# Performance work log

Hardware: AMD Instinct MI355X
Metric: run time of the kernel (lower is better)

The kernel has to match this reference:

```python
import jax, jax.numpy as jnp
import numpy as np

D_MODEL = 2048
N_HEADS = 16
HEAD_DIM = D_MODEL // N_HEADS


def setup_inputs() -> dict:
    key = jax.random.key(0)
    ks = jax.random.split(key, 5)
    scale = 1.0 / np.sqrt(D_MODEL)
    x = jax.random.normal(ks[0], (2, 2048, D_MODEL), dtype=jnp.float32)
    W_qkv = jax.random.normal(ks[1], (D_MODEL, 3 * D_MODEL), dtype=jnp.float32) * scale
    b_qkv = jnp.zeros((3 * D_MODEL,), dtype=jnp.float32)
    W_out = jax.random.normal(ks[2], (D_MODEL, D_MODEL), dtype=jnp.float32) * scale
    b_out = jnp.zeros((D_MODEL,), dtype=jnp.float32)
    return {"x": x, "W_qkv": W_qkv, "b_qkv": b_qkv, "W_out": W_out, "b_out": b_out}


def reference(x, W_qkv, b_qkv, W_out, b_out):
    bsz, seq_len, _ = x.shape
    # QKV projection: (b, s, 3*d) -> (3, b, h, s, hd)
    qkv = x @ W_qkv + b_qkv
    qkv = qkv.reshape(bsz, seq_len, 3, N_HEADS, HEAD_DIM)
    qkv = jnp.transpose(qkv, (2, 0, 3, 1, 4))
    q, k, v = qkv[0], qkv[1], qkv[2]
    # scaled dot-product scores: (b, h, s, s)
    scores = jnp.einsum("bhqd,bhkd->bhqk", q, k) / np.sqrt(HEAD_DIM).astype(np.float32)
    causal = jnp.tril(jnp.ones((seq_len, seq_len), dtype=bool))
    scores = jnp.where(causal[None, None], scores, -jnp.inf)
    attn = jax.nn.softmax(scores, axis=-1)
    # attention output: (b, h, s, hd) -> (b, s, d)
    out = jnp.einsum("bhqk,bhkd->bhqd", attn, v)
    out = jnp.transpose(out, (0, 2, 1, 3)).reshape(bsz, seq_len, D_MODEL)
    y = out @ W_out + b_out
    return y
```

## Files before the change

### kernel.cpp

```cpp
#include <hip/hip_runtime.h>
#include <stdint.h>
#include <stddef.h>


typedef __attribute__((ext_vector_type(8))) short bf16x8;
typedef __attribute__((ext_vector_type(4))) float f32x4;

#define SOFT_SCALE 0.12751743075419806f

__device__ __forceinline__ short f2bf(float f) {
  union { float f; unsigned u; } v; v.f = f;
  unsigned u = v.u + 0x7fffu + ((v.u >> 16) & 1u);
  return (short)(u >> 16);
}

__device__ __forceinline__ void gload_lds16(const void* g, const void* l) {
  __builtin_amdgcn_global_load_lds(
      (__attribute__((address_space(1))) void*)(uintptr_t)g,
      (__attribute__((address_space(3))) void*)(uintptr_t)l,
      16, 0, 0);
}

__global__ __launch_bounds__(256) void cast_f32_bf16(
    const float* __restrict__ in, short* __restrict__ out, int n8) {
  int i = blockIdx.x * 256 + threadIdx.x;
  if (i >= n8) return;
  float4 a = ((const float4*)in)[i * 2];
  float4 b = ((const float4*)in)[i * 2 + 1];
  bf16x8 o;
  o[0] = f2bf(a.x); o[1] = f2bf(a.y); o[2] = f2bf(a.z); o[3] = f2bf(a.w);
  o[4] = f2bf(b.x); o[5] = f2bf(b.y); o[6] = f2bf(b.z); o[7] = f2bf(b.w);
  ((bf16x8*)out)[i] = o;
}

__global__ __launch_bounds__(256) void transpose_cast_w(
    const float* __restrict__ W, short* __restrict__ WT, int K, int N) {
  __shared__ short t[32][33];
  int k0 = blockIdx.x * 32, n0 = blockIdx.y * 32;
  int r = threadIdx.x >> 3;
  int c = (threadIdx.x & 7) * 4;
  float4 v = *(const float4*)(W + (size_t)(k0 + r) * N + n0 + c);
  t[r][c + 0] = f2bf(v.x); t[r][c + 1] = f2bf(v.y);
  t[r][c + 2] = f2bf(v.z); t[r][c + 3] = f2bf(v.w);
  __syncthreads();
  short4 o;
  o.x = t[c + 0][r]; o.y = t[c + 1][r]; o.z = t[c + 2][r]; o.w = t[c + 3][r];
  *(short4*)(WT + (size_t)(n0 + r) * K + k0 + c) = o;
}

template <int BF16OUT, int VTRANS, int QSCALE>
__global__ __launch_bounds__(512, 2) void gemm256(
    const short* __restrict__ A, const short* __restrict__ BT,
    void* __restrict__ Cv, const float* __restrict__ bias,
    short* __restrict__ vTout, int M, int N, int K) {
  (void)M;
  __shared__ __align__(16) short SH[73728];
  const int tid = threadIdx.x;
  const int wave = tid >> 6, lane = tid & 63;
  const int quad = lane >> 4, l16 = lane & 15;
  const int wm = wave >> 1, wn = wave & 1;
  const int kx = (l16 & 7) << 3;

  const int gx = gridDim.x;
  int bid = blockIdx.y * gx + blockIdx.x;
  const int nwg = gx * gridDim.y;
  bid = (bid & 7) * (nwg >> 3) + (bid >> 3);
  const int m0 = (bid % gx) * 256, n0 = (bid / gx) * 128;

  const int rsub = lane >> 3;
  const int csub = ((lane & 7) ^ rsub) << 3;
  const short* aS[4];
  const short* bS[2];
#pragma unroll
  for (int i = 0; i < 4; ++i)
    aS[i] = A + (size_t)(m0 + (wave * 4 + i) * 8 + rsub) * K + csub;
#pragma unroll
  for (int i = 0; i < 2; ++i)
    bS[i] = BT + (size_t)(n0 + (wave * 2 + i) * 8 + rsub) * K + csub;

  auto stageA = [&](int st, int sb) {
#pragma unroll
    for (int i = 0; i < 4; ++i)
      gload_lds16(aS[i] + st * 64,
                  (const char*)SH + sb * 49152 + (wave * 4 + i) * 1024);
  };
  auto stageB = [&](int st, int sb) {
#pragma unroll
    for (int i = 0; i < 2; ++i)
      gload_lds16(bS[i] + st * 64,
                  (const char*)SH + sb * 49152 + 32768 + (wave * 2 + i) * 1024);
  };

  stageA(0, 0); stageB(0, 0);
  stageA(1, 1); stageB(1, 1);

  f32x4 acc[4][4] = {};
  const int nT = K >> 6;
  int buf = 0, sb = 2;
  for (int t = 0; t < nT; ++t) {
    const int st = (t + 2 < nT) ? (t + 2) : (nT - 1);
    const short* As = (const short*)((const char*)SH + buf * 49152);
    const short* Bs = As + 16384;

    asm volatile("s_waitcnt vmcnt(6)" ::: "memory");
    __builtin_amdgcn_s_barrier();

    bf16x8 af[4][2], bf[2][2];
#pragma unroll
    for (int f = 0; f < 4; ++f) {
      const int row = wm * 64 + f * 16 + l16;
#pragma unroll
      for (int kk = 0; kk < 2; ++kk)
        af[f][kk] = *(const bf16x8*)(As + row * 64 +
                                     (((kk << 5) | (quad << 3)) ^ kx));
    }
#pragma unroll
    for (int u = 0; u < 2; ++u) {
      const int row = wn * 64 + u * 16 + l16;
#pragma unroll
      for (int kk = 0; kk < 2; ++kk)
        bf[u][kk] = *(const bf16x8*)(Bs + row * 64 +
                                     (((kk << 5) | (quad << 3)) ^ kx));
    }
    stageA(st, sb);
    __builtin_amdgcn_s_barrier();
    asm volatile("s_waitcnt lgkmcnt(0)" ::: "memory");
    __builtin_amdgcn_sched_barrier(0);
    __builtin_amdgcn_s_setprio(1);
#pragma unroll
    for (int f = 0; f < 4; ++f)
#pragma unroll
      for (int u = 0; u < 2; ++u)
#pragma unroll
        for (int kk = 0; kk < 2; ++kk)
          acc[f][u] = __builtin_amdgcn_mfma_f32_16x16x32_bf16(
              af[f][kk], bf[u][kk], acc[f][u], 0, 0, 0);
    __builtin_amdgcn_s_setprio(0);
    __builtin_amdgcn_s_barrier();

#pragma unroll
    for (int u = 0; u < 2; ++u) {
      const int row = wn * 64 + 32 + u * 16 + l16;
#pragma unroll
      for (int kk = 0; kk < 2; ++kk)
        bf[u][kk] = *(const bf16x8*)(Bs + row * 64 +
                                     (((kk << 5) | (quad << 3)) ^ kx));
    }
    stageB(st, sb);
    __builtin_amdgcn_s_barrier();
    asm volatile("s_waitcnt lgkmcnt(0)" ::: "memory");
    __builtin_amdgcn_sched_barrier(0);
    __builtin_amdgcn_s_setprio(1);
#pragma unroll
    for (int f = 0; f < 4; ++f)
#pragma unroll
      for (int u = 0; u < 2; ++u)
#pragma unroll
        for (int kk = 0; kk < 2; ++kk)
          acc[f][2 + u] = __builtin_amdgcn_mfma_f32_16x16x32_bf16(
              af[f][kk], bf[u][kk], acc[f][2 + u], 0, 0, 0);
    __builtin_amdgcn_s_setprio(0);

    buf = (buf == 2) ? 0 : buf + 1;
    sb = (sb == 2) ? 0 : sb + 1;
  }

  if (VTRANS && n0 >= 4096) {
    asm volatile("s_waitcnt vmcnt(0)" ::: "memory");
    __builtin_amdgcn_s_barrier();
    short* T = (short*)SH;
#pragma unroll
    for (int j = 0; j < 4; ++j) {
      const int nl = wn * 64 + j * 16 + l16;
      const float bv = bias[n0 + nl];
#pragma unroll
      for (int f = 0; f < 4; ++f) {
        const int ml = wm * 64 + f * 16 + quad * 4;
        short4 o;
        o.x = f2bf(acc[f][j][0] + bv);
        o.y = f2bf(acc[f][j][1] + bv);
        o.z = f2bf(acc[f][j][2] + bv);
        o.w = f2bf(acc[f][j][3] + bv);
        *(short4*)(T + nl * 264 + ml) = o;
      }
    }
    __builtin_amdgcn_s_barrier();
    const int b = m0 >> 11, s0 = m0 & 2047, h = (n0 - 4096) >> 7;
#pragma unroll
    for (int pass = 0; pass < 8; ++pass) {
      const int row = pass * 16 + (tid >> 5);
      const int c = (tid & 31) * 8;
      bf16x8 v = *(const bf16x8*)(T + row * 264 + c);
      *(bf16x8*)(vTout + ((size_t)((b * 16 + h) * 128 + row)) * 2048 + s0 +
                 c) = v;
    }
    return;
  }

#pragma unroll
  for (int j = 0; j < 4; ++j) {
    const int n = n0 + wn * 64 + j * 16 + l16;
    const float bv = bias[n];
#pragma unroll
    for (int f = 0; f < 4; ++f) {
      const int mb = m0 + wm * 64 + f * 16 + quad * 4;
#pragma unroll
      for (int r = 0; r < 4; ++r) {
        float v = acc[f][j][r] + bv;
        if (QSCALE && n < 2048) v *= SOFT_SCALE;
        if (BF16OUT)
          ((short*)Cv)[(size_t)(mb + r) * N + n] = f2bf(v);
        else
          ((float*)Cv)[(size_t)(mb + r) * N + n] = v;
      }
    }
  }
}

__global__ __launch_bounds__(512, 4) void attn_kernel(
    const short* __restrict__ qkv, const short* __restrict__ vT,
    short* __restrict__ obuf) {
  __shared__ __align__(16) short Ks[2 * 8192];
  __shared__ __align__(16) short Vs[2 * 8192];
  __shared__ __align__(16) short Ps[8192];
  const int tid = threadIdx.x;
  const int wave = tid >> 6, lane = tid & 63;
  const int quad = lane >> 4, l16 = lane & 15;
  const int bh = blockIdx.y, b = bh >> 4, h = bh & 15;
  const int px = blockIdx.x;
  const int p = (blockIdx.y & 16) ? (15 - px) : px;
  const int q0 = p * 128;
  const int nkt = 2 * (p + 1);

  const short* qbase = qkv + (size_t)b * 2048 * 6144 + h * 128;
  const short* kbase = qkv + (size_t)b * 2048 * 6144 + 2048 + h * 128;
  const short* vtbase = vT + (size_t)bh * 128 * 2048;
  short* obase = obuf + (size_t)b * 2048 * 2048 + h * 128;

  const int srow = lane >> 2;
  const int scol = (lane & 3) * 8;

  bf16x8 ones;
#pragma unroll
  for (int j = 0; j < 8; ++j) ones[j] = (short)0x3F80;

  bf16x8 qf[4];
#pragma unroll
  for (int kk = 0; kk < 4; ++kk)
    qf[kk] = *(const bf16x8*)(
        qbase + (size_t)(q0 + wave * 16 + l16) * 6144 + kk * 32 + quad * 8);

  f32x4 acco[8] = {};
  f32x4 accl = {};

  auto stage = [&](int buf, int kt) {
    const int k0 = kt * 64;
#pragma unroll
    for (int it = 0; it < 2; ++it) {
      int c = wave * 2 + it;
      gload_lds16(
          kbase + (size_t)(k0 + (c & 3) * 16 + srow) * 6144 + (c >> 2) * 32 +
              scol,
          (const char*)Ks + buf * 16384 + c * 1024);
    }
#pragma unroll
    for (int it = 0; it < 2; ++it) {
      int c = wave * 2 + it;
      gload_lds16(
          vtbase + (size_t)((c & 7) * 16 + srow) * 2048 + k0 + (c >> 3) * 32 +
              scol,
          (const char*)Vs + buf * 16384 + c * 1024);
    }
  };

  stage(0, 0);

  for (int kt = 0; kt < nkt; ++kt) {
    const int buf = kt & 1;
    __syncthreads();
    if (kt + 1 < nkt) stage(1 - buf, kt + 1);
    const short* KsB = Ks + buf * 8192;
    const short* VsB = Vs + buf * 8192;

    f32x4 accs[4] = {};
#pragma unroll
    for (int kk = 0; kk < 4; ++kk) {
      bf16x8 bfg[4];
#pragma unroll
      for (int tn = 0; tn < 4; ++tn)
        bfg[tn] = *(const bf16x8*)(KsB + (kk * 4 + tn) * 512 + l16 * 32 +
                                   quad * 8);
#pragma unroll
      for (int tn = 0; tn < 4; ++tn)
        accs[tn] = __builtin_amdgcn_mfma_f32_16x16x32_bf16(
            qf[kk], bfg[tn], accs[tn], 0, 0, 0);
    }

    if (kt >= nkt - 2) {
      const int k0 = kt * 64;
#pragma unroll
      for (int tn = 0; tn < 4; ++tn)
#pragma unroll
        for (int r = 0; r < 4; ++r) {
          int grow = q0 + wave * 16 + quad * 4 + r;
          int gcol = k0 + tn * 16 + l16;
          if (gcol > grow) accs[tn][r] = -1e30f;
        }
    }
#pragma unroll
    for (int tn = 0; tn < 4; ++tn)
#pragma unroll
      for (int r = 0; r < 4; ++r) accs[tn][r] = exp2f(accs[tn][r]);

#pragma unroll
    for (int r = 0; r < 4; ++r)
#pragma unroll
      for (int tn = 0; tn < 4; ++tn)
        Ps[wave * 1024 + (tn >> 1) * 512 + (quad * 4 + r) * 32 +
           (tn & 1) * 16 + l16] = f2bf(accs[tn][r]);

#pragma unroll
    for (int kk2 = 0; kk2 < 2; ++kk2) {
      bf16x8 av = *(const bf16x8*)(Ps + wave * 1024 + kk2 * 512 + l16 * 32 +
                                   quad * 8);
      accl = __builtin_amdgcn_mfma_f32_16x16x32_bf16(av, ones, accl, 0, 0, 0);
      bf16x8 bfg[8];
#pragma unroll
      for (int tn = 0; tn < 8; ++tn)
        bfg[tn] = *(const bf16x8*)(VsB + (kk2 * 8 + tn) * 512 + l16 * 32 +
                                   quad * 8);
#pragma unroll
      for (int tn = 0; tn < 8; ++tn)
        acco[tn] = __builtin_amdgcn_mfma_f32_16x16x32_bf16(
            av, bfg[tn], acco[tn], 0, 0, 0);
    }
  }

  float inv[4];
#pragma unroll
  for (int r = 0; r < 4; ++r) inv[r] = 1.f / accl[r];
#pragma unroll
  for (int r = 0; r < 4; ++r) {
    int row = q0 + wave * 16 + quad * 4 + r;
#pragma unroll
    for (int tn = 0; tn < 8; ++tn)
      obase[(size_t)row * 2048 + tn * 16 + l16] = f2bf(acco[tn][r] * inv[r]);
  }
}

extern "C" void kernel_launch(void* const* d_in, const int* in_sizes, int n_in,
                              void* d_out, int out_size, void* d_ws,
                              size_t ws_size, hipStream_t stream) {
  (void)in_sizes; (void)n_in; (void)out_size; (void)ws_size;
  const float* x    = (const float*)d_in[0];
  const float* Wqkv = (const float*)d_in[1];
  const float* bqkv = (const float*)d_in[2];
  const float* Wout = (const float*)d_in[3];
  const float* bout = (const float*)d_in[4];
  float* out = (float*)d_out;

  char* ws = (char*)d_ws;
  short* xb    = (short*)(ws);
  short* wqkvT = (short*)(ws + 16777216);
  short* woutT = (short*)(ws + 41943040);
  short* qkv   = (short*)(ws + 50331648);
  short* vTb   = (short*)(ws + 100663296);
  short* obuf  = (short*)(ws + 117440512);

  cast_f32_bf16<<<4096, 256, 0, stream>>>(x, xb, 1048576);
  transpose_cast_w<<<dim3(64, 192), 256, 0, stream>>>(Wqkv, wqkvT, 2048, 6144);
  transpose_cast_w<<<dim3(64, 64), 256, 0, stream>>>(Wout, woutT, 2048, 2048);

  gemm256<1, 1, 1><<<dim3(16, 48), 512, 0, stream>>>(
      xb, wqkvT, (void*)qkv, bqkv, vTb, 4096, 6144, 2048);

  attn_kernel<<<dim3(16, 32), 512, 0, stream>>>(qkv, vTb, obuf);

  gemm256<0, 0, 0><<<dim3(16, 16), 512, 0, stream>>>(
      obuf, woutT, (void*)out, bout, nullptr, 4096, 2048, 2048);
}
```

Baseline: 363.6 us.

## Give each attention wave two query row groups and XOR-swizzle LDS tiles

```diff
diff --git a/kernel.cpp b/kernel.cpp
--- a/kernel.cpp
+++ b/kernel.cpp
@@ -217,7 +217,7 @@
   }
 }
 
-__global__ __launch_bounds__(512, 4) void attn_kernel(
+__global__ __launch_bounds__(256, 2) void attn_kernel(
     const short* __restrict__ qkv, const short* __restrict__ vT,
     short* __restrict__ obuf) {
   __shared__ __align__(16) short Ks[2 * 8192];
@@ -238,34 +238,38 @@
   short* obase = obuf + (size_t)b * 2048 * 2048 + h * 128;
 
   const int srow = lane >> 2;
-  const int scol = (lane & 3) * 8;
+  const int scol = ((lane & 3) ^ (srow & 3)) * 8;
+  const int kx = ((l16 & 3) << 3);
 
   bf16x8 ones;
 #pragma unroll
   for (int j = 0; j < 8; ++j) ones[j] = (short)0x3F80;
 
-  bf16x8 qf[4];
-#pragma unroll
-  for (int kk = 0; kk < 4; ++kk)
-    qf[kk] = *(const bf16x8*)(
-        qbase + (size_t)(q0 + wave * 16 + l16) * 6144 + kk * 32 + quad * 8);
-
-  f32x4 acco[8] = {};
-  f32x4 accl = {};
+  bf16x8 qf[2][4];
+#pragma unroll
+  for (int rg = 0; rg < 2; ++rg)
+#pragma unroll
+    for (int kk = 0; kk < 4; ++kk)
+      qf[rg][kk] = *(const bf16x8*)(
+          qbase + (size_t)(q0 + wave * 32 + rg * 16 + l16) * 6144 + kk * 32 +
+          quad * 8);
+
+  f32x4 acco[2][8] = {};
+  f32x4 accl[2] = {};
 
   auto stage = [&](int buf, int kt) {
     const int k0 = kt * 64;
 #pragma unroll
-    for (int it = 0; it < 2; ++it) {
-      int c = wave * 2 + it;
+    for (int it = 0; it < 4; ++it) {
+      int c = wave * 4 + it;
       gload_lds16(
           kbase + (size_t)(k0 + (c & 3) * 16 + srow) * 6144 + (c >> 2) * 32 +
               scol,
           (const char*)Ks + buf * 16384 + c * 1024);
     }
 #pragma unroll
-    for (int it = 0; it < 2; ++it) {
-      int c = wave * 2 + it;
+    for (int it = 0; it < 4; ++it) {
+      int c = wave * 4 + it;
       gload_lds16(
           vtbase + (size_t)((c & 7) * 16 + srow) * 2048 + k0 + (c >> 3) * 32 +
               scol,
@@ -282,70 +286,90 @@
     const short* KsB = Ks + buf * 8192;
     const short* VsB = Vs + buf * 8192;
 
-    f32x4 accs[4] = {};
+    f32x4 accs[2][4] = {};
 #pragma unroll
     for (int kk = 0; kk < 4; ++kk) {
       bf16x8 bfg[4];
 #pragma unroll
       for (int tn = 0; tn < 4; ++tn)
         bfg[tn] = *(const bf16x8*)(KsB + (kk * 4 + tn) * 512 + l16 * 32 +
-                                   quad * 8);
-#pragma unroll
-      for (int tn = 0; tn < 4; ++tn)
-        accs[tn] = __builtin_amdgcn_mfma_f32_16x16x32_bf16(
-            qf[kk], bfg[tn], accs[tn], 0, 0, 0);
+                                   ((quad * 8) ^ kx));
+#pragma unroll
+      for (int rg = 0; rg < 2; ++rg)
+#pragma unroll
+        for (int tn = 0; tn < 4; ++tn)
+          accs[rg][tn] = __builtin_amdgcn_mfma_f32_16x16x32_bf16(
+              qf[rg][kk], bfg[tn], accs[rg][tn], 0, 0, 0);
     }
 
     if (kt >= nkt - 2) {
       const int k0 = kt * 64;
 #pragma unroll
+      for (int rg = 0; rg < 2; ++rg)
+#pragma unroll
+        for (int tn = 0; tn < 4; ++tn)
+#pragma unroll
+          for (int r = 0; r < 4; ++r) {
+            int grow = q0 + wave * 32 + rg * 16 + quad * 4 + r;
+            int gcol = k0 + tn * 16 + l16;
+            if (gcol > grow) accs[rg][tn][r] = -1e30f;
+          }
+    }
+#pragma unroll
+    for (int rg = 0; rg < 2; ++rg)
+#pragma unroll
       for (int tn = 0; tn < 4; ++tn)
 #pragma unroll
-        for (int r = 0; r < 4; ++r) {
-          int grow = q0 + wave * 16 + quad * 4 + r;
-          int gcol = k0 + tn * 16 + l16;
-          if (gcol > grow) accs[tn][r] = -1e30f;
+        for (int r = 0; r < 4; ++r) accs[rg][tn][r] = exp2f(accs[rg][tn][r]);
+
+#pragma unroll
+    for (int rg = 0; rg < 2; ++rg)
+#pragma unroll
+      for (int r = 0; r < 4; ++r)
+#pragma unroll
+        for (int tn = 0; tn < 4; ++tn) {
+          const int row = rg * 16 + quad * 4 + r;
+          const int col = (tn & 1) * 16 + l16;
+          const int pcol = (col & 7) | ((((col >> 3) ^ row) & 3) << 3);
+          Ps[wave * 2048 + (tn >> 1) * 1024 + row * 32 + pcol] =
+              f2bf(accs[rg][tn][r]);
         }
-    }
-#pragma unroll
-    for (int tn = 0; tn < 4; ++tn)
-#pragma unroll
-      for (int r = 0; r < 4; ++r) accs[tn][r] = exp2f(accs[tn][r]);
-
-#pragma unroll
-    for (int r = 0; r < 4; ++r)
-#pragma unroll
-      for (int tn = 0; tn < 4; ++tn)
-        Ps[wave * 1024 + (tn >> 1) * 512 + (quad * 4 + r) * 32 +
-           (tn & 1) * 16 + l16] = f2bf(accs[tn][r]);
 
 #pragma unroll
     for (int kk2 = 0; kk2 < 2; ++kk2) {
-      bf16x8 av = *(const bf16x8*)(Ps + wave * 1024 + kk2 * 512 + l16 * 32 +
-                                   quad * 8);
-      accl = __builtin_amdgcn_mfma_f32_16x16x32_bf16(av, ones, accl, 0, 0, 0);
+      bf16x8 av[2];
+#pragma unroll
+      for (int rg = 0; rg < 2; ++rg)
+        av[rg] = *(const bf16x8*)(Ps + wave * 2048 + kk2 * 1024 +
+                                  (rg * 16 + l16) * 32 + ((quad * 8) ^ kx));
+#pragma unroll
+      for (int rg = 0; rg < 2; ++rg)
+        accl[rg] = __builtin_amdgcn_mfma_f32_16x16x32_bf16(av[rg], ones,
+                                                           accl[rg], 0, 0, 0);
       bf16x8 bfg[8];
 #pragma unroll
       for (int tn = 0; tn < 8; ++tn)
         bfg[tn] = *(const bf16x8*)(VsB + (kk2 * 8 + tn) * 512 + l16 * 32 +
-                                   quad * 8);
+                                   ((quad * 8) ^ kx));
 #pragma unroll
       for (int tn = 0; tn < 8; ++tn)
-        acco[tn] = __builtin_amdgcn_mfma_f32_16x16x32_bf16(
-            av, bfg[tn], acco[tn], 0, 0, 0);
+#pragma unroll
+        for (int rg = 0; rg < 2; ++rg)
+          acco[rg][tn] = __builtin_amdgcn_mfma_f32_16x16x32_bf16(
+              av[rg], bfg[tn], acco[rg][tn], 0, 0, 0);
     }
   }
 
-  float inv[4];
-#pragma unroll
-  for (int r = 0; r < 4; ++r) inv[r] = 1.f / accl[r];
-#pragma unroll
-  for (int r = 0; r < 4; ++r) {
-    int row = q0 + wave * 16 + quad * 4 + r;
-#pragma unroll
-    for (int tn = 0; tn < 8; ++tn)
-      obase[(size_t)row * 2048 + tn * 16 + l16] = f2bf(acco[tn][r] * inv[r]);
-  }
+#pragma unroll
+  for (int rg = 0; rg < 2; ++rg)
+#pragma unroll
+    for (int r = 0; r < 4; ++r) {
+      const float inv = 1.f / accl[rg][r];
+      const int row = q0 + wave * 32 + rg * 16 + quad * 4 + r;
+#pragma unroll
+      for (int tn = 0; tn < 8; ++tn)
+        obase[(size_t)row * 2048 + tn * 16 + l16] = f2bf(acco[rg][tn][r] * inv);
+    }
 }
 
 extern "C" void kernel_launch(void* const* d_in, const int* in_sizes, int n_in,
@@ -374,7 +398,7 @@
   gemm256<1, 1, 1><<<dim3(16, 48), 512, 0, stream>>>(
       xb, wqkvT, (void*)qkv, bqkv, vTb, 4096, 6144, 2048);
 
-  attn_kernel<<<dim3(16, 32), 512, 0, stream>>>(qkv, vTb, obuf);
+  attn_kernel<<<dim3(16, 32), 256, 0, stream>>>(qkv, vTb, obuf);
 
   gemm256<0, 0, 0><<<dim3(16, 16), 512, 0, stream>>>(
       obuf, woutT, (void*)out, bout, nullptr, 4096, 2048, 2048);
```

Measured after the change: 369.1 us. No clear change (+1.5%).

## Use dedicated 256x256-tile QKV GEMM with double-buffered staged loads

Applied to the files above, without the earlier changes.

```diff
diff --git a/kernel.cpp b/kernel.cpp
--- a/kernel.cpp
+++ b/kernel.cpp
@@ -48,11 +48,218 @@
   *(short4*)(WT + (size_t)(n0 + r) * K + k0 + c) = o;
 }
 
-template <int BF16OUT, int VTRANS, int QSCALE>
-__global__ __launch_bounds__(512, 2) void gemm256(
+__global__ __launch_bounds__(512, 2) void gemm_qkv(
     const short* __restrict__ A, const short* __restrict__ BT,
-    void* __restrict__ Cv, const float* __restrict__ bias,
+    short* __restrict__ C, const float* __restrict__ bias,
     short* __restrict__ vTout, int M, int N, int K) {
+  (void)M;
+  __shared__ __align__(16) short SH[66048];
+  const int tid = threadIdx.x;
+  const int wave = tid >> 6, lane = tid & 63;
+  const int quad = lane >> 4, l16 = lane & 15;
+  const int wm = wave >> 2, wn = wave & 3;
+  const int kx = (l16 & 7) << 3;
+
+  const int gx = gridDim.x;
+  int bid = blockIdx.y * gx + blockIdx.x;
+  const int nwg = gx * gridDim.y;
+  bid = (bid & 7) * (nwg >> 3) + (bid >> 3);
+  const int m0 = (bid % gx) * 256, n0 = (bid / gx) * 256;
+
+  const int rsub = lane >> 3;
+  const int csub = ((lane & 7) ^ rsub) << 3;
+  const int e1 = (wave & 3) + 8 * (wave >> 2);
+  const int cA[4] = {wave, wave + 16, wave + 8, wave + 24};
+  const int cB[4] = {e1, e1 + 16, e1 + 4, e1 + 20};
+  const short* aP[4];
+  const short* bP[4];
+#pragma unroll
+  for (int i = 0; i < 4; ++i) {
+    aP[i] = A + (size_t)(m0 + cA[i] * 8 + rsub) * K + csub;
+    bP[i] = BT + (size_t)(n0 + cB[i] * 8 + rsub) * K + csub;
+  }
+
+  auto stage = [&](int h, int st, int sbuf) {
+    if (h == 0 || h == 2) {
+      int i0 = (h == 0) ? 0 : 2;
+#pragma unroll
+      for (int i = 0; i < 2; ++i)
+        gload_lds16(aP[i0 + i] + st * 64,
+                    (const char*)SH + sbuf * 65536 + cA[i0 + i] * 1024);
+    } else {
+      int i0 = (h == 1) ? 0 : 2;
+#pragma unroll
+      for (int i = 0; i < 2; ++i)
+        gload_lds16(bP[i0 + i] + st * 64,
+                    (const char*)SH + sbuf * 65536 + 32768 + cB[i0 + i] * 1024);
+    }
+  };
+
+  stage(0, 0, 0); stage(1, 0, 0); stage(2, 0, 0); stage(3, 0, 0);
+
+  f32x4 acc[8][4] = {};
+  const int nT = K >> 6;
+  for (int t = 0; t < nT; ++t) {
+    const int st = (t + 1 < nT) ? (t + 1) : (nT - 1);
+    const int sbuf = (t + 1) & 1;
+    const short* As = SH + (t & 1) * 32768;
+    const short* Bs = As + 16384;
+    bf16x8 bf[4][2];
+
+    asm volatile("s_waitcnt vmcnt(4)" ::: "memory");
+    __builtin_amdgcn_s_barrier();
+    bf16x8 af0[4][2];
+#pragma unroll
+    for (int f = 0; f < 4; ++f) {
+      const int row = wm * 128 + f * 16 + l16;
+#pragma unroll
+      for (int kk = 0; kk < 2; ++kk)
+        af0[f][kk] = *(const bf16x8*)(As + row * 64 +
+                                      (((kk << 5) | (quad << 3)) ^ kx));
+    }
+#pragma unroll
+    for (int u = 0; u < 2; ++u) {
+      const int row = wn * 64 + u * 16 + l16;
+#pragma unroll
+      for (int kk = 0; kk < 2; ++kk)
+        bf[u][kk] = *(const bf16x8*)(Bs + row * 64 +
+                                     (((kk << 5) | (quad << 3)) ^ kx));
+    }
+    stage(0, st, sbuf);
+    __builtin_amdgcn_s_barrier();
+    asm volatile("s_waitcnt lgkmcnt(0)" ::: "memory");
+    __builtin_amdgcn_sched_barrier(0);
+    __builtin_amdgcn_s_setprio(1);
+#pragma unroll
+    for (int f = 0; f < 4; ++f)
+#pragma unroll
+      for (int u = 0; u < 2; ++u)
+#pragma unroll
+        for (int kk = 0; kk < 2; ++kk)
+          acc[f][u] = __builtin_amdgcn_mfma_f32_16x16x32_bf16(
+              af0[f][kk], bf[u][kk], acc[f][u], 0, 0, 0);
+    __builtin_amdgcn_s_setprio(0);
+
+    asm volatile("s_waitcnt vmcnt(2)" ::: "memory");
+    __builtin_amdgcn_s_barrier();
+#pragma unroll
+    for (int u = 0; u < 2; ++u) {
+      const int row = wn * 64 + 32 + u * 16 + l16;
+#pragma unroll
+      for (int kk = 0; kk < 2; ++kk)
+        bf[2 + u][kk] = *(const bf16x8*)(Bs + row * 64 +
+                                         (((kk << 5) | (quad << 3)) ^ kx));
+    }
+    stage(1, st, sbuf);
+    __builtin_amdgcn_s_barrier();
+    asm volatile("s_waitcnt lgkmcnt(0)" ::: "memory");
+    __builtin_amdgcn_sched_barrier(0);
+    __builtin_amdgcn_s_setprio(1);
+#pragma unroll
+    for (int f = 0; f < 4; ++f)
+#pragma unroll
+      for (int u = 0; u < 2; ++u)
+#pragma unroll
+        for (int kk = 0; kk < 2; ++kk)
+          acc[f][2 + u] = __builtin_amdgcn_mfma_f32_16x16x32_bf16(
+              af0[f][kk], bf[2 + u][kk], acc[f][2 + u], 0, 0, 0);
+    __builtin_amdgcn_s_setprio(0);
+
+    __builtin_amdgcn_s_barrier();
+    bf16x8 af1[4][2];
+#pragma unroll
+    for (int f = 0; f < 4; ++f) {
+      const int row = wm * 128 + 64 + f * 16 + l16;
+#pragma unroll
+      for (int kk = 0; kk < 2; ++kk)
+        af1[f][kk] = *(const bf16x8*)(As + row * 64 +
+                                      (((kk << 5) | (quad << 3)) ^ kx));
+    }
+    stage(2, st, sbuf);
+    __builtin_amdgcn_s_barrier();
+    asm volatile("s_waitcnt lgkmcnt(0)" ::: "memory");
+    __builtin_amdgcn_sched_barrier(0);
+    __builtin_amdgcn_s_setprio(1);
+#pragma unroll
+    for (int f = 0; f < 4; ++f)
+#pragma unroll
+      for (int u = 0; u < 2; ++u)
+#pragma unroll
+        for (int kk = 0; kk < 2; ++kk)
+          acc[4 + f][u] = __builtin_amdgcn_mfma_f32_16x16x32_bf16(
+              af1[f][kk], bf[u][kk], acc[4 + f][u], 0, 0, 0);
+    __builtin_amdgcn_s_setprio(0);
+
+    __builtin_amdgcn_s_barrier();
+    stage(3, st, sbuf);
+    __builtin_amdgcn_s_setprio(1);
+#pragma unroll
+    for (int f = 0; f < 4; ++f)
+#pragma unroll
+      for (int u = 0; u < 2; ++u)
+#pragma unroll
+        for (int kk = 0; kk < 2; ++kk)
+          acc[4 + f][2 + u] = __builtin_amdgcn_mfma_f32_16x16x32_bf16(
+              af1[f][kk], bf[2 + u][kk], acc[4 + f][2 + u], 0, 0, 0);
+    __builtin_amdgcn_s_setprio(0);
+  }
+
+  asm volatile("s_waitcnt vmcnt(0)" ::: "memory");
+  __builtin_amdgcn_s_barrier();
+
+  if (n0 >= 4096) {
+    short* T = (short*)SH;
+#pragma unroll
+    for (int j = 0; j < 4; ++j) {
+      const int nl = wn * 64 + j * 16 + l16;
+      const float bv = bias[n0 + nl];
+#pragma unroll
+      for (int f = 0; f < 8; ++f) {
+        const int ml = wm * 128 + f * 16 + quad * 4;
+        short4 o;
+        o.x = f2bf(acc[f][j][0] + bv);
+        o.y = f2bf(acc[f][j][1] + bv);
+        o.z = f2bf(acc[f][j][2] + bv);
+        o.w = f2bf(acc[f][j][3] + bv);
+        *(short4*)(T + nl * 258 + ml) = o;
+      }
+    }
+    __builtin_amdgcn_s_barrier();
+    const int b = m0 >> 11, s0 = m0 & 2047, h0 = (n0 - 4096) >> 7;
+#pragma unroll
+    for (int pass = 0; pass < 16; ++pass) {
+      const int nl = pass * 16 + (tid >> 5);
+      const int c = (tid & 31) * 8;
+      bf16x8 v = *(const bf16x8*)(T + nl * 258 + c);
+      *(bf16x8*)(vTout +
+                 ((size_t)((b * 16 + h0 + (nl >> 7)) * 128 + (nl & 127))) *
+                     2048 +
+                 s0 + c) = v;
+    }
+    return;
+  }
+
+#pragma unroll
+  for (int j = 0; j < 4; ++j) {
+    const int n = n0 + wn * 64 + j * 16 + l16;
+    const float bv = bias[n];
+#pragma unroll
+    for (int f = 0; f < 8; ++f) {
+      const int mb = m0 + wm * 128 + f * 16 + quad * 4;
+#pragma unroll
+      for (int r = 0; r < 4; ++r) {
+        float v = acc[f][j][r] + bv;
+        if (n < 2048) v *= SOFT_SCALE;
+        C[(size_t)(mb + r) * N + n] = f2bf(v);
+      }
+    }
+  }
+}
+
+__global__ __launch_bounds__(512, 2) void gemm_out(
+    const short* __restrict__ A, const short* __restrict__ BT,
+    float* __restrict__ C, const float* __restrict__ bias, int M, int N,
+    int K) {
   (void)M;
   __shared__ __align__(16) short SH[73728];
   const int tid = threadIdx.x;
@@ -165,37 +372,7 @@
     sb = (sb == 2) ? 0 : sb + 1;
   }
 
-  if (VTRANS && n0 >= 4096) {
-    asm volatile("s_waitcnt vmcnt(0)" ::: "memory");
-    __builtin_amdgcn_s_barrier();
-    short* T = (short*)SH;
-#pragma unroll
-    for (int j = 0; j < 4; ++j) {
-      const int nl = wn * 64 + j * 16 + l16;
-      const float bv = bias[n0 + nl];
-#pragma unroll
-      for (int f = 0; f < 4; ++f) {
-        const int ml = wm * 64 + f * 16 + quad * 4;
-        short4 o;
-        o.x = f2bf(acc[f][j][0] + bv);
-        o.y = f2bf(acc[f][j][1] + bv);
-        o.z = f2bf(acc[f][j][2] + bv);
-        o.w = f2bf(acc[f][j][3] + bv);
-        *(short4*)(T + nl * 264 + ml) = o;
-      }
-    }
-    __builtin_amdgcn_s_barrier();
-    const int b = m0 >> 11, s0 = m0 & 2047, h = (n0 - 4096) >> 7;
-#pragma unroll
-    for (int pass = 0; pass < 8; ++pass) {
-      const int row = pass * 16 + (tid >> 5);
-      const int c = (tid & 31) * 8;
-      bf16x8 v = *(const bf16x8*)(T + row * 264 + c);
-      *(bf16x8*)(vTout + ((size_t)((b * 16 + h) * 128 + row)) * 2048 + s0 +
-                 c) = v;
-    }
-    return;
-  }
+  asm volatile("s_waitcnt vmcnt(0)" ::: "memory");
 
 #pragma unroll
   for (int j = 0; j < 4; ++j) {
@@ -205,14 +382,8 @@
     for (int f = 0; f < 4; ++f) {
       const int mb = m0 + wm * 64 + f * 16 + quad * 4;
 #pragma unroll
-      for (int r = 0; r < 4; ++r) {
-        float v = acc[f][j][r] + bv;
-        if (QSCALE && n < 2048) v *= SOFT_SCALE;
-        if (BF16OUT)
-          ((short*)Cv)[(size_t)(mb + r) * N + n] = f2bf(v);
-        else
-          ((float*)Cv)[(size_t)(mb + r) * N + n] = v;
-      }
+      for (int r = 0; r < 4; ++r)
+        C[(size_t)(mb + r) * N + n] = acc[f][j][r] + bv;
     }
   }
 }
@@ -371,11 +542,11 @@
   transpose_cast_w<<<dim3(64, 192), 256, 0, stream>>>(Wqkv, wqkvT, 2048, 6144);
   transpose_cast_w<<<dim3(64, 64), 256, 0, stream>>>(Wout, woutT, 2048, 2048);
 
-  gemm256<1, 1, 1><<<dim3(16, 48), 512, 0, stream>>>(
-      xb, wqkvT, (void*)qkv, bqkv, vTb, 4096, 6144, 2048);
+  gemm_qkv<<<dim3(16, 24), 512, 0, stream>>>(
+      xb, wqkvT, qkv, bqkv, vTb, 4096, 6144, 2048);
 
   attn_kernel<<<dim3(16, 32), 512, 0, stream>>>(qkv, vTb, obuf);
 
-  gemm256<0, 0, 0><<<dim3(16, 16), 512, 0, stream>>>(
-      obuf, woutT, (void*)out, bout, nullptr, 4096, 2048, 2048);
-}
+  gemm_out<<<dim3(16, 16), 512, 0, stream>>>(
+      obuf, woutT, out, bout, 4096, 2048, 2048);
+}
```

New measurement: 373.0 us. 2.6% more time.

## Triple-buffer attention K/V tiles with 32-key steps and vmcnt-based waits

Applied to the files above, without the earlier changes.

```diff
diff --git a/kernel.cpp b/kernel.cpp
--- a/kernel.cpp
+++ b/kernel.cpp
@@ -197,6 +197,8 @@
     return;
   }
 
+  asm volatile("s_waitcnt vmcnt(0)" ::: "memory");
+
 #pragma unroll
   for (int j = 0; j < 4; ++j) {
     const int n = n0 + wn * 64 + j * 16 + l16;
@@ -220,9 +222,9 @@
 __global__ __launch_bounds__(512, 4) void attn_kernel(
     const short* __restrict__ qkv, const short* __restrict__ vT,
     short* __restrict__ obuf) {
-  __shared__ __align__(16) short Ks[2 * 8192];
-  __shared__ __align__(16) short Vs[2 * 8192];
-  __shared__ __align__(16) short Ps[8192];
+  __shared__ __align__(16) short Ks[3 * 4096];
+  __shared__ __align__(16) short Vs[3 * 4096];
+  __shared__ __align__(16) short Ps[4096];
   const int tid = threadIdx.x;
   const int wave = tid >> 6, lane = tid & 63;
   const int quad = lane >> 4, l16 = lane & 15;
@@ -230,7 +232,7 @@
   const int px = blockIdx.x;
   const int p = (blockIdx.y & 16) ? (15 - px) : px;
   const int q0 = p * 128;
-  const int nkt = 2 * (p + 1);
+  const int nkt = 4 * (p + 1);
 
   const short* qbase = qkv + (size_t)b * 2048 * 6144 + h * 128;
   const short* kbase = qkv + (size_t)b * 2048 * 6144 + 2048 + h * 128;
@@ -253,53 +255,48 @@
   f32x4 acco[8] = {};
   f32x4 accl = {};
 
-  auto stage = [&](int buf, int kt) {
-    const int k0 = kt * 64;
-#pragma unroll
-    for (int it = 0; it < 2; ++it) {
-      int c = wave * 2 + it;
-      gload_lds16(
-          kbase + (size_t)(k0 + (c & 3) * 16 + srow) * 6144 + (c >> 2) * 32 +
-              scol,
-          (const char*)Ks + buf * 16384 + c * 1024);
-    }
-#pragma unroll
-    for (int it = 0; it < 2; ++it) {
-      int c = wave * 2 + it;
-      gload_lds16(
-          vtbase + (size_t)((c & 7) * 16 + srow) * 2048 + k0 + (c >> 3) * 32 +
-              scol,
-          (const char*)Vs + buf * 16384 + c * 1024);
-    }
+  auto stage = [&](int sb, int kt) {
+    const int k0 = kt * 32;
+    gload_lds16(
+        kbase + (size_t)(k0 + (wave & 1) * 16 + srow) * 6144 +
+            (wave >> 1) * 32 + scol,
+        (const char*)Ks + sb * 8192 + wave * 1024);
+    gload_lds16(
+        vtbase + (size_t)(wave * 16 + srow) * 2048 + k0 + scol,
+        (const char*)Vs + sb * 8192 + wave * 1024);
   };
 
   stage(0, 0);
-
+  stage(1, 1);
+
+  int buf = 0;
   for (int kt = 0; kt < nkt; ++kt) {
-    const int buf = kt & 1;
-    __syncthreads();
-    if (kt + 1 < nkt) stage(1 - buf, kt + 1);
-    const short* KsB = Ks + buf * 8192;
-    const short* VsB = Vs + buf * 8192;
-
-    f32x4 accs[4] = {};
+    const int st = (kt + 2 < nkt) ? (kt + 2) : (nkt - 1);
+    asm volatile("s_waitcnt vmcnt(2)" ::: "memory");
+    __builtin_amdgcn_s_barrier();
+    const int sbn = (buf >= 1) ? buf - 1 : 2;
+    stage(sbn, st);
+    const short* KsB = Ks + buf * 4096;
+    const short* VsB = Vs + buf * 4096;
+
+    f32x4 accs[2] = {};
 #pragma unroll
     for (int kk = 0; kk < 4; ++kk) {
-      bf16x8 bfg[4];
-#pragma unroll
-      for (int tn = 0; tn < 4; ++tn)
-        bfg[tn] = *(const bf16x8*)(KsB + (kk * 4 + tn) * 512 + l16 * 32 +
+      bf16x8 bfg[2];
+#pragma unroll
+      for (int tn = 0; tn < 2; ++tn)
+        bfg[tn] = *(const bf16x8*)(KsB + (kk * 2 + tn) * 512 + l16 * 32 +
                                    quad * 8);
 #pragma unroll
-      for (int tn = 0; tn < 4; ++tn)
+      for (int tn = 0; tn < 2; ++tn)
         accs[tn] = __builtin_amdgcn_mfma_f32_16x16x32_bf16(
             qf[kk], bfg[tn], accs[tn], 0, 0, 0);
     }
 
-    if (kt >= nkt - 2) {
-      const int k0 = kt * 64;
-#pragma unroll
-      for (int tn = 0; tn < 4; ++tn)
+    if (kt >= nkt - 4) {
+      const int k0 = kt * 32;
+#pragma unroll
+      for (int tn = 0; tn < 2; ++tn)
 #pragma unroll
         for (int r = 0; r < 4; ++r) {
           int grow = q0 + wave * 16 + quad * 4 + r;
@@ -308,33 +305,32 @@
         }
     }
 #pragma unroll
-    for (int tn = 0; tn < 4; ++tn)
+    for (int tn = 0; tn < 2; ++tn)
 #pragma unroll
       for (int r = 0; r < 4; ++r) accs[tn][r] = exp2f(accs[tn][r]);
 
 #pragma unroll
     for (int r = 0; r < 4; ++r)
 #pragma unroll
-      for (int tn = 0; tn < 4; ++tn)
-        Ps[wave * 1024 + (tn >> 1) * 512 + (quad * 4 + r) * 32 +
-           (tn & 1) * 16 + l16] = f2bf(accs[tn][r]);
-
-#pragma unroll
-    for (int kk2 = 0; kk2 < 2; ++kk2) {
-      bf16x8 av = *(const bf16x8*)(Ps + wave * 1024 + kk2 * 512 + l16 * 32 +
-                                   quad * 8);
-      accl = __builtin_amdgcn_mfma_f32_16x16x32_bf16(av, ones, accl, 0, 0, 0);
-      bf16x8 bfg[8];
-#pragma unroll
-      for (int tn = 0; tn < 8; ++tn)
-        bfg[tn] = *(const bf16x8*)(VsB + (kk2 * 8 + tn) * 512 + l16 * 32 +
-                                   quad * 8);
-#pragma unroll
-      for (int tn = 0; tn < 8; ++tn)
-        acco[tn] = __builtin_amdgcn_mfma_f32_16x16x32_bf16(
-            av, bfg[tn], acco[tn], 0, 0, 0);
-    }
-  }
+      for (int tn = 0; tn < 2; ++tn)
+        Ps[wave * 512 + (quad * 4 + r) * 32 + tn * 16 + l16] =
+            f2bf(accs[tn][r]);
+
+    bf16x8 av = *(const bf16x8*)(Ps + wave * 512 + l16 * 32 + quad * 8);
+    accl = __builtin_amdgcn_mfma_f32_16x16x32_bf16(av, ones, accl, 0, 0, 0);
+    bf16x8 bfg[8];
+#pragma unroll
+    for (int tn = 0; tn < 8; ++tn)
+      bfg[tn] = *(const bf16x8*)(VsB + tn * 512 + l16 * 32 + quad * 8);
+#pragma unroll
+    for (int tn = 0; tn < 8; ++tn)
+      acco[tn] = __builtin_amdgcn_mfma_f32_16x16x32_bf16(
+          av, bfg[tn], acco[tn], 0, 0, 0);
+
+    buf = (buf == 2) ? 0 : buf + 1;
+  }
+
+  asm volatile("s_waitcnt vmcnt(0)" ::: "memory");
 
   float inv[4];
 #pragma unroll
```

Result: no change. 363.9 us (+0.1%).
